# Performance work log

Measured on AMD Instinct MI355X. Metric: run time of the kernel, lower is better.

The kernel has to match this reference:

```python
import jax, jax.numpy as jnp
import numpy as np

N_NODES = 100000
N_EDGES = 3200000
IN_FEATS, N_HIDDEN, OUT_FEATS = 256, 128, 40


def setup_inputs() -> dict:
    key = jax.random.key(0)
    ks = jax.random.split(key, 8)
    x = jax.random.normal(ks[0], (N_NODES, IN_FEATS), dtype=jnp.float32)
    W0 = jax.random.normal(ks[1], (IN_FEATS, N_HIDDEN), dtype=jnp.float32) * (1.0 / np.sqrt(IN_FEATS))
    b0 = jnp.zeros((N_HIDDEN,), dtype=jnp.float32)
    W1 = jax.random.normal(ks[2], (N_HIDDEN, OUT_FEATS), dtype=jnp.float32) * (1.0 / np.sqrt(N_HIDDEN))
    b1 = jnp.zeros((OUT_FEATS,), dtype=jnp.float32)
    edge_weight = jax.random.uniform(ks[3], (N_EDGES,), dtype=jnp.float32)
    src = jax.random.randint(ks[4], (N_EDGES,), 0, N_NODES)
    dst = jax.random.randint(ks[5], (N_EDGES,), 0, N_NODES)
    return {"x": x, "W0": W0, "b0": b0, "W1": W1, "b1": b1,
            "edge_weight": edge_weight, "src": src, "dst": dst}


def reference(x, W0, b0, W1, b1, edge_weight, src, dst):
    n_nodes = x.shape[0]

    def gcn_conv(h, W, b):
        # linear transform first (PyG-style GCNConv), then sparse aggregate (SpMM)
        h = h @ W                                  # [N, d_out]
        msg = h[src] * edge_weight[:, None]        # [E, d_out] gathered + scaled
        agg = jax.ops.segment_sum(msg, dst, num_segments=n_nodes)  # scatter-add
        return agg + b

    h = jax.nn.relu(gcn_conv(x, W0, b0))
    out = gcn_conv(h, W1, b1)
    return jax.nn.log_softmax(out, axis=1)
```

## Files before the change

kernel.cpp:

```cpp
#include <hip/hip_runtime.h>
#include <hip/hip_bf16.h>
#include <cstdint>
#include <cstddef>

#define N_NODES   100000
#define N_EDGES   3200000
#define IN_FEATS  256
#define N_HIDDEN  128
#define OUT_FEATS 40

#define NB        196
#define EPB       8192
#define NBLK      391
#define HIST_M    (NB * NBLK)
#define N_TILES   3125
#define TPB       2
#define G0BLKS    ((N_TILES + TPB - 1) / TPB)

typedef __attribute__((ext_vector_type(8))) __bf16 bf16x8;
typedef __attribute__((ext_vector_type(4))) float f32x4;

#define ACC8(A_, V_, W_)                                                  \
  A_[0] = fmaf(__uint_as_float((V_).x << 16),         (W_), A_[0]);       \
  A_[1] = fmaf(__uint_as_float((V_).x & 0xFFFF0000u), (W_), A_[1]);       \
  A_[2] = fmaf(__uint_as_float((V_).y << 16),         (W_), A_[2]);       \
  A_[3] = fmaf(__uint_as_float((V_).y & 0xFFFF0000u), (W_), A_[3]);       \
  A_[4] = fmaf(__uint_as_float((V_).z << 16),         (W_), A_[4]);       \
  A_[5] = fmaf(__uint_as_float((V_).z & 0xFFFF0000u), (W_), A_[5]);       \
  A_[6] = fmaf(__uint_as_float((V_).w << 16),         (W_), A_[6]);       \
  A_[7] = fmaf(__uint_as_float((V_).w & 0xFFFF0000u), (W_), A_[7]);

__device__ __forceinline__ void gemm0_block(
    int bid, const float* __restrict__ x, const uint4* __restrict__ w0f,
    unsigned short* __restrict__ h0) {
  __shared__ __align__(16) unsigned short xb[32 * 264];
  const int tid  = threadIdx.x;
  const int lane = tid & 63;
  const int wave = tid >> 6;
  const int rb   = wave & 1;
  const int ch   = wave >> 1;
  const int l15  = lane & 15;
  const int g    = lane >> 4;

  bf16x8 Bf[4][8];
#pragma unroll
  for (int cb = 0; cb < 4; ++cb)
#pragma unroll
    for (int q = 0; q < 8; ++q)
      Bf[cb][q] = __builtin_bit_cast(bf16x8, w0f[((ch * 4 + cb) * 8 + q) * 64 + lane]);

  for (int t = 0; t < TPB; ++t) {
    const int tile = bid * TPB + t;
    if (tile >= N_TILES) break;
    const int row0 = tile * 32;
    __syncthreads();
    for (int i = tid; i < 32 * 128; i += 256) {
      const int row = i >> 7, kp = i & 127;
      const float2 v = *(const float2*)(x + (size_t)(row0 + row) * IN_FEATS + kp * 2);
      __hip_bfloat162 p;
      p.x = __float2bfloat16(v.x);
      p.y = __float2bfloat16(v.y);
      *(unsigned int*)&xb[row * 264 + kp * 2] = *(unsigned int*)&p;
    }
    __syncthreads();

    f32x4 acc[4];
#pragma unroll
    for (int cb = 0; cb < 4; ++cb) acc[cb] = (f32x4){0.f, 0.f, 0.f, 0.f};

#pragma unroll
    for (int q = 0; q < 8; ++q) {
      const bf16x8 a = *(const bf16x8*)&xb[(rb * 16 + l15) * 264 + q * 32 + g * 8];
      acc[0] = __builtin_amdgcn_mfma_f32_16x16x32_bf16(a, Bf[0][q], acc[0], 0, 0, 0);
      acc[1] = __builtin_amdgcn_mfma_f32_16x16x32_bf16(a, Bf[1][q], acc[1], 0, 0, 0);
      acc[2] = __builtin_amdgcn_mfma_f32_16x16x32_bf16(a, Bf[2][q], acc[2], 0, 0, 0);
      acc[3] = __builtin_amdgcn_mfma_f32_16x16x32_bf16(a, Bf[3][q], acc[3], 0, 0, 0);
    }

#pragma unroll
    for (int cb = 0; cb < 4; ++cb) {
      const int col = ch * 64 + cb * 16 + l15;
#pragma unroll
      for (int r = 0; r < 4; ++r) {
        const int row = row0 + rb * 16 + g * 4 + r;
        __hip_bfloat16 hb = __float2bfloat16(acc[cb][r]);
        h0[(size_t)row * N_HIDDEN + col] = *(unsigned short*)&hb;
      }
    }
  }
}

__device__ __forceinline__ void bucket_scan_block(
    int b, const int* __restrict__ bsum, int* __restrict__ histG) {
  __shared__ int sh[256];
  __shared__ int pr[256];
  const int t = threadIdx.x;

  sh[t] = (t < b) ? bsum[t] : 0;
  __syncthreads();
#pragma unroll
  for (int off = 128; off > 0; off >>= 1) {
    if (t < off) sh[t] += sh[t + off];
    __syncthreads();
  }
  const int base = sh[0];

  const int row = b * NBLK;
  const int i0 = 2 * t, i1 = 2 * t + 1;
  int a = 0, c = 0;
  if (t < 196) {
    a = histG[row + i0];
    if (i1 < NBLK) c = histG[row + i1];
  }
  pr[t] = a + c;
  __syncthreads();
  for (int off = 1; off < 256; off <<= 1) {
    int v = (t >= off) ? pr[t - off] : 0;
    __syncthreads();
    pr[t] += v;
    __syncthreads();
  }
  if (t < 196) {
    const int ebase = (t > 0) ? pr[t - 1] : 0;
    histG[row + i0] = base + ebase;
    if (i1 < NBLK) histG[row + i1] = base + ebase + a;
  }
}

__global__ __launch_bounds__(256) void bscan_gemm0_kernel(
    const int* __restrict__ bsum, int* __restrict__ histG,
    const float* __restrict__ x, const uint4* __restrict__ w0f,
    unsigned short* __restrict__ h0) {
  if (blockIdx.x < NB) bucket_scan_block(blockIdx.x, bsum, histG);
  else                 gemm0_block(blockIdx.x - NB, x, w0f, h0);
}

__global__ __launch_bounds__(256) void p1hist_kernel(
    const int* __restrict__ dst, int* __restrict__ histG,
    const float* __restrict__ W1, uint4* __restrict__ w1f,
    const float* __restrict__ W0, uint4* __restrict__ w0f,
    int* __restrict__ bsum) {
  const int tid = threadIdx.x;
  const int blk = blockIdx.x;

  if (blk >= NBLK) {
    if (blk == NBLK) {
      for (int t = tid; t < 3 * 4 * 64; t += 256) {
        const int ln  = t & 63;
        const int qq  = (t >> 6) & 3;
        const int nt  = t >> 8;
        const int l15 = ln & 15;
        const int gg  = ln >> 4;
        const int c   = nt * 16 + l15;
        const int k0  = qq * 32 + gg * 8;
        uint4 u;
        __hip_bfloat162 p;
#define W1AT(i_) ((c < OUT_FEATS) ? W1[(size_t)(k0 + (i_)) * OUT_FEATS + c] : 0.f)
        p.x = __float2bfloat16(W1AT(0)); p.y = __float2bfloat16(W1AT(1));
        u.x = *(unsigned int*)&p;
        p.x = __float2bfloat16(W1AT(2)); p.y = __float2bfloat16(W1AT(3));
        u.y = *(unsigned int*)&p;
        p.x = __float2bfloat16(W1AT(4)); p.y = __float2bfloat16(W1AT(5));
        u.z = *(unsigned int*)&p;
        p.x = __float2bfloat16(W1AT(6)); p.y = __float2bfloat16(W1AT(7));
        u.w = *(unsigned int*)&p;
#undef W1AT
        w1f[t] = u;
      }
    } else {
      const int pb = blk - NBLK - 1;
      for (int fi = pb * 512 + tid; fi < pb * 512 + 512; fi += 256) {
        const int ln  = fi & 63;
        const int qq  = (fi >> 6) & 7;
        const int ct  = fi >> 9;
        const int col = ct * 16 + (ln & 15);
        const int k0  = qq * 32 + (ln >> 4) * 8;
        uint4 u;
        __hip_bfloat162 p;
        p.x = __float2bfloat16(W0[(size_t)(k0 + 0) * N_HIDDEN + col]);
        p.y = __float2bfloat16(W0[(size_t)(k0 + 1) * N_HIDDEN + col]);
        u.x = *(unsigned int*)&p;
        p.x = __float2bfloat16(W0[(size_t)(k0 + 2) * N_HIDDEN + col]);
        p.y = __float2bfloat16(W0[(size_t)(k0 + 3) * N_HIDDEN + col]);
        u.y = *(unsigned int*)&p;
        p.x = __float2bfloat16(W0[(size_t)(k0 + 4) * N_HIDDEN + col]);
        p.y = __float2bfloat16(W0[(size_t)(k0 + 5) * N_HIDDEN + col]);
        u.z = *(unsigned int*)&p;
        p.x = __float2bfloat16(W0[(size_t)(k0 + 6) * N_HIDDEN + col]);
        p.y = __float2bfloat16(W0[(size_t)(k0 + 7) * N_HIDDEN + col]);
        u.w = *(unsigned int*)&p;
        w0f[fi] = u;
      }
    }
    return;
  }

  __shared__ int lh[NB];
  for (int i = tid; i < NB; i += 256) lh[i] = 0;
  __syncthreads();

  const int e0 = blk * EPB;
  const int e1 = min(e0 + EPB, N_EDGES);
  for (int i = e0 + tid; i < e1; i += 256)
    atomicAdd(&lh[dst[i] >> 9], 1);
  __syncthreads();

  for (int i = tid; i < NB; i += 256) {
    histG[i * NBLK + blk] = lh[i];
    atomicAdd(&bsum[i], lh[i]);
  }
}

__global__ __launch_bounds__(256) void p1scatter_kernel(
    const int* __restrict__ src, const int* __restrict__ dst,
    const float* __restrict__ ew, const int* __restrict__ histG,
    uint2* __restrict__ bucketed) {
  __shared__ uint2 stage[EPB];
  __shared__ unsigned char sbkt[EPB];
  __shared__ int lcnt[NB];
  __shared__ int lbase[NB];
  __shared__ int spart[256];
  const int tid = threadIdx.x;
  const int blk = blockIdx.x;
  const int e0 = blk * EPB;
  const int e1 = min(e0 + EPB, N_EDGES);

  for (int i = tid; i < NB; i += 256) lcnt[i] = 0;
  __syncthreads();

  for (int i = e0 + tid; i < e1; i += 256)
    atomicAdd(&lcnt[dst[i] >> 9], 1);
  __syncthreads();

  const int myv = (tid < NB) ? lcnt[tid] : 0;
  spart[tid] = myv;
  __syncthreads();
  for (int off = 1; off < 256; off <<= 1) {
    int u = (tid >= off) ? spart[tid - off] : 0;
    __syncthreads();
    spart[tid] += u;
    __syncthreads();
  }
  if (tid < NB) { lbase[tid] = spart[tid] - myv; lcnt[tid] = spart[tid] - myv; }
  __syncthreads();

  for (int i = e0 + tid; i < e1; i += 256) {
    const int d = dst[i];
    const int b = d >> 9;
    const int pos = atomicAdd(&lcnt[b], 1);
    stage[pos] = make_uint2((unsigned)src[i] | ((unsigned)(d & 511) << 17),
                            __float_as_uint(ew[i]));
    sbkt[pos] = (unsigned char)b;
  }
  __syncthreads();

  const int n = e1 - e0;
  for (int i = tid; i < n; i += 256) {
    const int b = sbkt[i];
    const int gpos = histG[b * NBLK + blk] + (i - lbase[b]);
    bucketed[gpos] = stage[i];
  }
}

__global__ __launch_bounds__(256) void p2place_kernel(
    const uint2* __restrict__ bucketed, const int* __restrict__ histG,
    int* __restrict__ offsets, int2* __restrict__ srcw) {
  __shared__ int cnt[512];
  __shared__ int part[256];
  const int t = threadIdx.x;
  const int b = blockIdx.x;
  const int node0 = b << 9;
  const int beg = histG[b * NBLK];
  const int end = (b == NB - 1) ? N_EDGES : histG[(b + 1) * NBLK];

  cnt[t] = 0; cnt[t + 256] = 0;
  __syncthreads();

  for (int j = beg + t; j < end; j += 256)
    atomicAdd(&cnt[bucketed[j].x >> 17], 1);
  __syncthreads();

  const int a0 = cnt[2 * t];
  const int a1 = cnt[2 * t + 1];
  part[t] = a0 + a1;
  __syncthreads();
  for (int off = 1; off < 256; off <<= 1) {
    int v = (t >= off) ? part[t - off] : 0;
    __syncthreads();
    part[t] += v;
    __syncthreads();
  }
  const int base = (t > 0) ? part[t - 1] : 0;

  const int o0 = beg + base;
  const int o1 = o0 + a0;
  cnt[2 * t]     = o0;
  cnt[2 * t + 1] = o1;
  const int n0 = node0 + 2 * t;
  if (n0 < N_NODES)     offsets[n0]     = o0;
  if (n0 + 1 < N_NODES) offsets[n0 + 1] = o1;
  if (b == NB - 1 && t == 0) offsets[N_NODES] = N_EDGES;
  __syncthreads();

  for (int j = beg + t; j < end; j += 256) {
    const uint2 en = bucketed[j];
    const int slot = atomicAdd(&cnt[en.x >> 17], 1);
    srcw[slot] = make_int2((int)(en.x & 0x1FFFFu), (int)en.y);
  }
}

__global__ __launch_bounds__(256) void gather0_gemm1_kernel(
    const uint4* __restrict__ h0q, const int2* __restrict__ srcw,
    const int* __restrict__ offsets, const float* __restrict__ b0,
    const uint4* __restrict__ w1f, unsigned short* __restrict__ h1a,
    unsigned short* __restrict__ h1c) {
  __shared__ float hs[4][N_HIDDEN];
  const int wave = threadIdx.x >> 6;
  const int lane = threadIdx.x & 63;
  const int node = blockIdx.x * 4 + wave;
  const int q    = lane >> 4;
  const int fl   = lane & 15;

  const int beg = __builtin_amdgcn_readfirstlane(offsets[node]);
  const int end = __builtin_amdgcn_readfirstlane(offsets[node + 1]);

  float acc[8] = {0.f, 0.f, 0.f, 0.f, 0.f, 0.f, 0.f, 0.f};

  if (end > beg) {
    const int e1 = end - 1;
    int2 sA = srcw[min(beg + q, e1)];
    int2 sB = srcw[min(beg + 4 + q, e1)];
    for (int j = beg; j < end; j += 8) {
      const float wA = (j + q < end)     ? __int_as_float(sA.y) : 0.f;
      const float wB = (j + 4 + q < end) ? __int_as_float(sB.y) : 0.f;
      const uint4 vA = h0q[(size_t)(unsigned)sA.x * 16 + fl];
      const uint4 vB = h0q[(size_t)(unsigned)sB.x * 16 + fl];
      const int jn = j + 8;
      if (jn < end) {
        sA = srcw[min(jn + q, e1)];
        sB = srcw[min(jn + 4 + q, e1)];
      }
      ACC8(acc, vA, wA)
      ACC8(acc, vB, wB)
    }
  }

#pragma unroll
  for (int i = 0; i < 8; ++i) {
    acc[i] += __shfl_xor(acc[i], 16);
    acc[i] += __shfl_xor(acc[i], 32);
  }

  if (q == 0) {
    const int f0 = fl * 8;
    float t[8];
#pragma unroll
    for (int i = 0; i < 8; ++i) {
      const float v = acc[i] + b0[f0 + i];
      t[i] = v > 0.f ? v : 0.f;
    }
    *(float4*)&hs[wave][f0]     = make_float4(t[0], t[1], t[2], t[3]);
    *(float4*)&hs[wave][f0 + 4] = make_float4(t[4], t[5], t[6], t[7]);
  }
  __syncthreads();

  if (wave < 3) {
    const int l15 = lane & 15;
    const int g   = lane >> 4;
    f32x4 c = {0.f, 0.f, 0.f, 0.f};
#pragma unroll
    for (int qq = 0; qq < 4; ++qq) {
      uint4 ua = make_uint4(0, 0, 0, 0);
      if (l15 < 4) {
        const float* hrow = &hs[l15][qq * 32 + g * 8];
        __hip_bfloat162 p;
        p.x = __float2bfloat16(hrow[0]); p.y = __float2bfloat16(hrow[1]);
        ua.x = *(unsigned int*)&p;
        p.x = __float2bfloat16(hrow[2]); p.y = __float2bfloat16(hrow[3]);
        ua.y = *(unsigned int*)&p;
        p.x = __float2bfloat16(hrow[4]); p.y = __float2bfloat16(hrow[5]);
        ua.z = *(unsigned int*)&p;
        p.x = __float2bfloat16(hrow[6]); p.y = __float2bfloat16(hrow[7]);
        ua.w = *(unsigned int*)&p;
      }
      const uint4 ub = w1f[(wave * 4 + qq) * 64 + lane];
      c = __builtin_amdgcn_mfma_f32_16x16x32_bf16(
            __builtin_bit_cast(bf16x8, ua), __builtin_bit_cast(bf16x8, ub),
            c, 0, 0, 0);
    }
    if (g == 0) {
#pragma unroll
      for (int r = 0; r < 4; ++r) {
        const int nodeR = blockIdx.x * 4 + r;
        const int f = wave * 16 + l15;
        __hip_bfloat16 hb = __float2bfloat16(c[r]);
        const unsigned short v16 = *(unsigned short*)&hb;
        if (f < 32)              h1a[(size_t)nodeR * 32 + f] = v16;
        else if (f < OUT_FEATS)  h1c[(size_t)nodeR * 8 + (f - 32)] = v16;
      }
    }
  }
}

__global__ __launch_bounds__(256) void gather1_lsm_kernel(
    const uint4* __restrict__ h1aq, const uint4* __restrict__ h1cq,
    const int2* __restrict__ srcw, const int* __restrict__ offsets,
    const float* __restrict__ b1, float* __restrict__ out) {
  const int wave = threadIdx.x >> 6;
  const int lane = threadIdx.x & 63;
  const int node = blockIdx.x * 4 + wave;
  const int g  = lane >> 2;
  const int fl = lane & 3;

  const int beg = __builtin_amdgcn_readfirstlane(offsets[node]);
  const int end = __builtin_amdgcn_readfirstlane(offsets[node + 1]);

  float acc[8]  = {0.f, 0.f, 0.f, 0.f, 0.f, 0.f, 0.f, 0.f};
  float acc2[8] = {0.f, 0.f, 0.f, 0.f, 0.f, 0.f, 0.f, 0.f};

  if (end > beg) {
    const int e1 = end - 1;
    int2 sA = srcw[min(beg + g, e1)];
    int2 sB = srcw[min(beg + 16 + g, e1)];
    for (int j = beg; j < end; j += 32) {
      const float wA = (j + g < end)      ? __int_as_float(sA.y) : 0.f;
      const float wB = (j + 16 + g < end) ? __int_as_float(sB.y) : 0.f;
      const uint4 vA = h1aq[(size_t)(unsigned)sA.x * 4 + fl];
      const uint4 vB = h1aq[(size_t)(unsigned)sB.x * 4 + fl];
      uint4 cA = make_uint4(0, 0, 0, 0), cB = make_uint4(0, 0, 0, 0);
      if (fl == 0) {
        cA = h1cq[(unsigned)sA.x];
        cB = h1cq[(unsigned)sB.x];
      }
      const int jn = j + 32;
      if (jn < end) {
        sA = srcw[min(jn + g, e1)];
        sB = srcw[min(jn + 16 + g, e1)];
      }
      ACC8(acc, vA, wA)
      ACC8(acc, vB, wB)
      if (fl == 0) {
        ACC8(acc2, cA, wA)
        ACC8(acc2, cB, wB)
      }
    }
  }

#pragma unroll
  for (int i = 0; i < 8; ++i) {
    acc[i]  += __shfl_xor(acc[i], 4);
    acc[i]  += __shfl_xor(acc[i], 8);
    acc[i]  += __shfl_xor(acc[i], 16);
    acc[i]  += __shfl_xor(acc[i], 32);
    acc2[i] += __shfl_xor(acc2[i], 4);
    acc2[i] += __shfl_xor(acc2[i], 8);
    acc2[i] += __shfl_xor(acc2[i], 16);
    acc2[i] += __shfl_xor(acc2[i], 32);
    acc2[i] += __shfl_xor(acc2[i], 1);
    acc2[i] += __shfl_xor(acc2[i], 2);
  }

  const int f0 = fl * 8;
  float m = -INFINITY;
#pragma unroll
  for (int i = 0; i < 8; ++i) {
    acc[i]  += b1[f0 + i];
    acc2[i] += b1[32 + i];
    m = fmaxf(m, acc[i]);
    m = fmaxf(m, acc2[i]);
  }
  m = fmaxf(m, __shfl_xor(m, 1));
  m = fmaxf(m, __shfl_xor(m, 2));

  float s = 0.f;
#pragma unroll
  for (int i = 0; i < 8; ++i) s += expf(acc[i] - m);
  s += __shfl_xor(s, 1);
  s += __shfl_xor(s, 2);
  float s2 = 0.f;
#pragma unroll
  for (int i = 0; i < 8; ++i) s2 += expf(acc2[i] - m);
  s += s2;

  const float lse = m + logf(s);
  if (lane < 4) {
    float* op = out + (size_t)node * OUT_FEATS + fl * 8;
    *(float4*)op       = make_float4(acc[0] - lse, acc[1] - lse,
                                     acc[2] - lse, acc[3] - lse);
    *(float4*)(op + 4) = make_float4(acc[4] - lse, acc[5] - lse,
                                     acc[6] - lse, acc[7] - lse);
  } else if (lane == 4) {
    float* op = out + (size_t)node * OUT_FEATS + 32;
    *(float4*)op       = make_float4(acc2[0] - lse, acc2[1] - lse,
                                     acc2[2] - lse, acc2[3] - lse);
    *(float4*)(op + 4) = make_float4(acc2[4] - lse, acc2[5] - lse,
                                     acc2[6] - lse, acc2[7] - lse);
  }
}

extern "C" void kernel_launch(void* const* d_in, const int* in_sizes, int n_in,
                              void* d_out, int out_size, void* d_ws, size_t ws_size,
                              hipStream_t stream) {
  const float* x   = (const float*)d_in[0];
  const float* W0  = (const float*)d_in[1];
  const float* b0  = (const float*)d_in[2];
  const float* W1  = (const float*)d_in[3];
  const float* b1  = (const float*)d_in[4];
  const float* ew  = (const float*)d_in[5];
  const int*   src = (const int*)d_in[6];
  const int*   dst = (const int*)d_in[7];
  float* out = (float*)d_out;

  char* ws = (char*)d_ws;
  unsigned int* h0b2 = (unsigned int*)(ws);
  int2*  srcw     = (int2*)(ws + 25600000);
  uint2* bucketed = (uint2*)(ws + 51200000);
  int*   offsets  = (int*)(ws + 76800000);
  int*   histG    = (int*)(ws + 77200064);
  unsigned short* h1a = (unsigned short*)(ws + 77506624);
  unsigned short* h1c = (unsigned short*)(ws + 83906624);
  uint4* w1f      = (uint4*)(ws + 85506624);
  uint4* w0f      = (uint4*)(ws + 85518912);
  int*   bsum     = (int*)(ws + 85584448);

  hipMemsetAsync(bsum, 0, NB * sizeof(int), stream);
  p1hist_kernel<<<NBLK + 9, 256, 0, stream>>>(dst, histG, W1, w1f, W0, w0f, bsum);
  bscan_gemm0_kernel<<<NB + G0BLKS, 256, 0, stream>>>(
      bsum, histG, x, w0f, (unsigned short*)h0b2);
  p1scatter_kernel<<<NBLK, 256, 0, stream>>>(src, dst, ew, histG, bucketed);
  p2place_kernel<<<NB, 256, 0, stream>>>(bucketed, histG, offsets, srcw);

  gather0_gemm1_kernel<<<N_NODES / 4, 256, 0, stream>>>(
      (const uint4*)h0b2, srcw, offsets, b0, (const uint4*)w1f, h1a, h1c);
  gather1_lsm_kernel<<<N_NODES / 4, 256, 0, stream>>>(
      (const uint4*)h1a, (const uint4*)h1c, srcw, offsets, b1, out);
}
```

Baseline: 511.2 us.

## Replace two-pass bucketed CSR build with global-atomic counting sort and packed FMA

Swaps the two-level bucket histogram/scatter/place CSR construction for a per-node global atomic histogram, a two-kernel node-level prefix scan, and a direct atomic-cursor scatter into the CSR edge array. This drops the intermediate bucketed buffer and one full pass over the edges, but relies on heavily contended global atomics and produces a nondeterministic edge order within each node. The gather kernels also switch to packed float2 FMAs, and the hidden-state LDS row is padded.

```diff
diff --git a/kernel.cpp b/kernel.cpp
--- a/kernel.cpp
+++ b/kernel.cpp
@@ -9,26 +9,28 @@
 #define N_HIDDEN  128
 #define OUT_FEATS 40
 
-#define NB        196
-#define EPB       8192
-#define NBLK      391
-#define HIST_M    (NB * NBLK)
+#define NCHUNK    391
+#define HISTB     391
 #define N_TILES   3125
 #define TPB       2
 #define G0BLKS    ((N_TILES + TPB - 1) / TPB)
 
 typedef __attribute__((ext_vector_type(8))) __bf16 bf16x8;
 typedef __attribute__((ext_vector_type(4))) float f32x4;
-
-#define ACC8(A_, V_, W_)                                                  \
-  A_[0] = fmaf(__uint_as_float((V_).x << 16),         (W_), A_[0]);       \
-  A_[1] = fmaf(__uint_as_float((V_).x & 0xFFFF0000u), (W_), A_[1]);       \
-  A_[2] = fmaf(__uint_as_float((V_).y << 16),         (W_), A_[2]);       \
-  A_[3] = fmaf(__uint_as_float((V_).y & 0xFFFF0000u), (W_), A_[3]);       \
-  A_[4] = fmaf(__uint_as_float((V_).z << 16),         (W_), A_[4]);       \
-  A_[5] = fmaf(__uint_as_float((V_).z & 0xFFFF0000u), (W_), A_[5]);       \
-  A_[6] = fmaf(__uint_as_float((V_).w << 16),         (W_), A_[6]);       \
-  A_[7] = fmaf(__uint_as_float((V_).w & 0xFFFF0000u), (W_), A_[7]);
+typedef __attribute__((ext_vector_type(2))) float f32x2;
+
+__device__ __forceinline__ void pkfma(f32x2& a, unsigned int u, f32x2 w2) {
+  f32x2 b;
+  b.x = __uint_as_float(u << 16);
+  b.y = __uint_as_float(u & 0xFFFF0000u);
+  a += b * w2;
+}
+
+#define ACC8P(A_, V_, W2_)   \
+  pkfma(A_[0], (V_).x, W2_); \
+  pkfma(A_[1], (V_).y, W2_); \
+  pkfma(A_[2], (V_).z, W2_); \
+  pkfma(A_[3], (V_).w, W2_);
 
 __device__ __forceinline__ void gemm0_block(
     int bid, const float* __restrict__ x, const uint4* __restrict__ w0f,
@@ -90,61 +92,15 @@
   }
 }
 
-__device__ __forceinline__ void bucket_scan_block(
-    int b, const int* __restrict__ bsum, int* __restrict__ histG) {
-  __shared__ int sh[256];
-  __shared__ int pr[256];
-  const int t = threadIdx.x;
-
-  sh[t] = (t < b) ? bsum[t] : 0;
-  __syncthreads();
-#pragma unroll
-  for (int off = 128; off > 0; off >>= 1) {
-    if (t < off) sh[t] += sh[t + off];
-    __syncthreads();
-  }
-  const int base = sh[0];
-
-  const int row = b * NBLK;
-  const int i0 = 2 * t, i1 = 2 * t + 1;
-  int a = 0, c = 0;
-  if (t < 196) {
-    a = histG[row + i0];
-    if (i1 < NBLK) c = histG[row + i1];
-  }
-  pr[t] = a + c;
-  __syncthreads();
-  for (int off = 1; off < 256; off <<= 1) {
-    int v = (t >= off) ? pr[t - off] : 0;
-    __syncthreads();
-    pr[t] += v;
-    __syncthreads();
-  }
-  if (t < 196) {
-    const int ebase = (t > 0) ? pr[t - 1] : 0;
-    histG[row + i0] = base + ebase;
-    if (i1 < NBLK) histG[row + i1] = base + ebase + a;
-  }
-}
-
-__global__ __launch_bounds__(256) void bscan_gemm0_kernel(
-    const int* __restrict__ bsum, int* __restrict__ histG,
-    const float* __restrict__ x, const uint4* __restrict__ w0f,
-    unsigned short* __restrict__ h0) {
-  if (blockIdx.x < NB) bucket_scan_block(blockIdx.x, bsum, histG);
-  else                 gemm0_block(blockIdx.x - NB, x, w0f, h0);
-}
-
-__global__ __launch_bounds__(256) void p1hist_kernel(
-    const int* __restrict__ dst, int* __restrict__ histG,
+__global__ __launch_bounds__(256) void hist_prep_kernel(
+    const int* __restrict__ dst, int* __restrict__ cnt,
     const float* __restrict__ W1, uint4* __restrict__ w1f,
-    const float* __restrict__ W0, uint4* __restrict__ w0f,
-    int* __restrict__ bsum) {
+    const float* __restrict__ W0, uint4* __restrict__ w0f) {
   const int tid = threadIdx.x;
   const int blk = blockIdx.x;
 
-  if (blk >= NBLK) {
-    if (blk == NBLK) {
+  if (blk >= HISTB) {
+    if (blk == HISTB) {
       for (int t = tid; t < 3 * 4 * 64; t += 256) {
         const int ln  = t & 63;
         const int qq  = (t >> 6) & 3;
@@ -168,7 +124,7 @@
         w1f[t] = u;
       }
     } else {
-      const int pb = blk - NBLK - 1;
+      const int pb = blk - HISTB - 1;
       for (int fi = pb * 512 + tid; fi < pb * 512 + 512; fi += 256) {
         const int ln  = fi & 63;
         const int qq  = (fi >> 6) & 7;
@@ -195,117 +151,78 @@
     return;
   }
 
-  __shared__ int lh[NB];
-  for (int i = tid; i < NB; i += 256) lh[i] = 0;
+#pragma unroll 4
+  for (int i = blk * 256 + tid; i < N_EDGES; i += HISTB * 256)
+    atomicAdd(&cnt[dst[i]], 1);
+}
+
+__global__ __launch_bounds__(256) void psum_kernel(
+    const int* __restrict__ cnt, int* __restrict__ psum) {
+  __shared__ int sh[256];
+  const int b = blockIdx.x, t = threadIdx.x;
+  const int n = b * 256 + t;
+  sh[t] = (n < N_NODES) ? cnt[n] : 0;
   __syncthreads();
-
-  const int e0 = blk * EPB;
-  const int e1 = min(e0 + EPB, N_EDGES);
-  for (int i = e0 + tid; i < e1; i += 256)
-    atomicAdd(&lh[dst[i] >> 9], 1);
+#pragma unroll
+  for (int off = 128; off > 0; off >>= 1) {
+    if (t < off) sh[t] += sh[t + off];
+    __syncthreads();
+  }
+  if (t == 0) psum[b] = sh[0];
+}
+
+__device__ __forceinline__ void node_scan_block(
+    int b, const int* __restrict__ cnt, const int* __restrict__ psum,
+    int* __restrict__ offsets, int* __restrict__ curs) {
+  __shared__ int sh[256];
+  __shared__ int pr[256];
+  const int t = threadIdx.x;
+
+  int v = (t < b) ? psum[t] : 0;
+  if (t + 256 < b) v += psum[t + 256];
+  sh[t] = v;
   __syncthreads();
-
-  for (int i = tid; i < NB; i += 256) {
-    histG[i * NBLK + blk] = lh[i];
-    atomicAdd(&bsum[i], lh[i]);
-  }
-}
-
-__global__ __launch_bounds__(256) void p1scatter_kernel(
-    const int* __restrict__ src, const int* __restrict__ dst,
-    const float* __restrict__ ew, const int* __restrict__ histG,
-    uint2* __restrict__ bucketed) {
-  __shared__ uint2 stage[EPB];
-  __shared__ unsigned char sbkt[EPB];
-  __shared__ int lcnt[NB];
-  __shared__ int lbase[NB];
-  __shared__ int spart[256];
-  const int tid = threadIdx.x;
-  const int blk = blockIdx.x;
-  const int e0 = blk * EPB;
-  const int e1 = min(e0 + EPB, N_EDGES);
-
-  for (int i = tid; i < NB; i += 256) lcnt[i] = 0;
-  __syncthreads();
-
-  for (int i = e0 + tid; i < e1; i += 256)
-    atomicAdd(&lcnt[dst[i] >> 9], 1);
-  __syncthreads();
-
-  const int myv = (tid < NB) ? lcnt[tid] : 0;
-  spart[tid] = myv;
+#pragma unroll
+  for (int off = 128; off > 0; off >>= 1) {
+    if (t < off) sh[t] += sh[t + off];
+    __syncthreads();
+  }
+  const int base = sh[0];
+
+  const int node = b * 256 + t;
+  const int c = (node < N_NODES) ? cnt[node] : 0;
+  pr[t] = c;
   __syncthreads();
   for (int off = 1; off < 256; off <<= 1) {
-    int u = (tid >= off) ? spart[tid - off] : 0;
-    __syncthreads();
-    spart[tid] += u;
-    __syncthreads();
-  }
-  if (tid < NB) { lbase[tid] = spart[tid] - myv; lcnt[tid] = spart[tid] - myv; }
-  __syncthreads();
-
-  for (int i = e0 + tid; i < e1; i += 256) {
+    int u = (t >= off) ? pr[t - off] : 0;
+    __syncthreads();
+    pr[t] += u;
+    __syncthreads();
+  }
+  const int excl = base + pr[t] - c;
+  if (node < N_NODES) { offsets[node] = excl; curs[node] = excl; }
+  if (b == NCHUNK - 1 && t == 255) offsets[N_NODES] = base + pr[255];
+}
+
+__global__ __launch_bounds__(256) void nscan_gemm0_kernel(
+    const int* __restrict__ cnt, const int* __restrict__ psum,
+    int* __restrict__ offsets, int* __restrict__ curs,
+    const float* __restrict__ x, const uint4* __restrict__ w0f,
+    unsigned short* __restrict__ h0) {
+  if (blockIdx.x < NCHUNK) node_scan_block(blockIdx.x, cnt, psum, offsets, curs);
+  else                     gemm0_block(blockIdx.x - NCHUNK, x, w0f, h0);
+}
+
+__global__ __launch_bounds__(256) void scatter_kernel(
+    const int* __restrict__ src, const int* __restrict__ dst,
+    const float* __restrict__ ew, int* __restrict__ curs,
+    int2* __restrict__ srcw) {
+#pragma unroll 4
+  for (int i = blockIdx.x * 256 + threadIdx.x; i < N_EDGES;
+       i += gridDim.x * 256) {
     const int d = dst[i];
-    const int b = d >> 9;
-    const int pos = atomicAdd(&lcnt[b], 1);
-    stage[pos] = make_uint2((unsigned)src[i] | ((unsigned)(d & 511) << 17),
-                            __float_as_uint(ew[i]));
-    sbkt[pos] = (unsigned char)b;
-  }
-  __syncthreads();
-
-  const int n = e1 - e0;
-  for (int i = tid; i < n; i += 256) {
-    const int b = sbkt[i];
-    const int gpos = histG[b * NBLK + blk] + (i - lbase[b]);
-    bucketed[gpos] = stage[i];
-  }
-}
-
-__global__ __launch_bounds__(256) void p2place_kernel(
-    const uint2* __restrict__ bucketed, const int* __restrict__ histG,
-    int* __restrict__ offsets, int2* __restrict__ srcw) {
-  __shared__ int cnt[512];
-  __shared__ int part[256];
-  const int t = threadIdx.x;
-  const int b = blockIdx.x;
-  const int node0 = b << 9;
-  const int beg = histG[b * NBLK];
-  const int end = (b == NB - 1) ? N_EDGES : histG[(b + 1) * NBLK];
-
-  cnt[t] = 0; cnt[t + 256] = 0;
-  __syncthreads();
-
-  for (int j = beg + t; j < end; j += 256)
-    atomicAdd(&cnt[bucketed[j].x >> 17], 1);
-  __syncthreads();
-
-  const int a0 = cnt[2 * t];
-  const int a1 = cnt[2 * t + 1];
-  part[t] = a0 + a1;
-  __syncthreads();
-  for (int off = 1; off < 256; off <<= 1) {
-    int v = (t >= off) ? part[t - off] : 0;
-    __syncthreads();
-    part[t] += v;
-    __syncthreads();
-  }
-  const int base = (t > 0) ? part[t - 1] : 0;
-
-  const int o0 = beg + base;
-  const int o1 = o0 + a0;
-  cnt[2 * t]     = o0;
-  cnt[2 * t + 1] = o1;
-  const int n0 = node0 + 2 * t;
-  if (n0 < N_NODES)     offsets[n0]     = o0;
-  if (n0 + 1 < N_NODES) offsets[n0 + 1] = o1;
-  if (b == NB - 1 && t == 0) offsets[N_NODES] = N_EDGES;
-  __syncthreads();
-
-  for (int j = beg + t; j < end; j += 256) {
-    const uint2 en = bucketed[j];
-    const int slot = atomicAdd(&cnt[en.x >> 17], 1);
-    srcw[slot] = make_int2((int)(en.x & 0x1FFFFu), (int)en.y);
+    const int pos = atomicAdd(&curs[d], 1);
+    srcw[pos] = make_int2(src[i], __float_as_int(ew[i]));
   }
 }
 
@@ -314,7 +231,7 @@
     const int* __restrict__ offsets, const float* __restrict__ b0,
     const uint4* __restrict__ w1f, unsigned short* __restrict__ h1a,
     unsigned short* __restrict__ h1c) {
-  __shared__ float hs[4][N_HIDDEN];
+  __shared__ float hs[4][132];
   const int wave = threadIdx.x >> 6;
   const int lane = threadIdx.x & 63;
   const int node = blockIdx.x * 4 + wave;
@@ -324,7 +241,9 @@
   const int beg = __builtin_amdgcn_readfirstlane(offsets[node]);
   const int end = __builtin_amdgcn_readfirstlane(offsets[node + 1]);
 
-  float acc[8] = {0.f, 0.f, 0.f, 0.f, 0.f, 0.f, 0.f, 0.f};
+  f32x2 acc[4];
+#pragma unroll
+  for (int i = 0; i < 4; ++i) acc[i] = (f32x2){0.f, 0.f};
 
   if (end > beg) {
     const int e1 = end - 1;
@@ -333,6 +252,8 @@
     for (int j = beg; j < end; j += 8) {
       const float wA = (j + q < end)     ? __int_as_float(sA.y) : 0.f;
       const float wB = (j + 4 + q < end) ? __int_as_float(sB.y) : 0.f;
+      const f32x2 w2A = {wA, wA};
+      const f32x2 w2B = {wB, wB};
       const uint4 vA = h0q[(size_t)(unsigned)sA.x * 16 + fl];
       const uint4 vB = h0q[(size_t)(unsigned)sB.x * 16 + fl];
       const int jn = j + 8;
@@ -340,15 +261,17 @@
         sA = srcw[min(jn + q, e1)];
         sB = srcw[min(jn + 4 + q, e1)];
       }
-      ACC8(acc, vA, wA)
-      ACC8(acc, vB, wB)
-    }
-  }
-
-#pragma unroll
-  for (int i = 0; i < 8; ++i) {
-    acc[i] += __shfl_xor(acc[i], 16);
-    acc[i] += __shfl_xor(acc[i], 32);
+      ACC8P(acc, vA, w2A)
+      ACC8P(acc, vB, w2B)
+    }
+  }
+
+#pragma unroll
+  for (int i = 0; i < 4; ++i) {
+    acc[i].x += __shfl_xor(acc[i].x, 16);
+    acc[i].x += __shfl_xor(acc[i].x, 32);
+    acc[i].y += __shfl_xor(acc[i].y, 16);
+    acc[i].y += __shfl_xor(acc[i].y, 32);
   }
 
   if (q == 0) {
@@ -356,7 +279,8 @@
     float t[8];
 #pragma unroll
     for (int i = 0; i < 8; ++i) {
-      const float v = acc[i] + b0[f0 + i];
+      const float a = ((i & 1) ? acc[i >> 1].y : acc[i >> 1].x);
+      const float v = a + b0[f0 + i];
       t[i] = v > 0.f ? v : 0.f;
     }
     *(float4*)&hs[wave][f0]     = make_float4(t[0], t[1], t[2], t[3]);
@@ -415,8 +339,9 @@
   const int beg = __builtin_amdgcn_readfirstlane(offsets[node]);
   const int end = __builtin_amdgcn_readfirstlane(offsets[node + 1]);
 
-  float acc[8]  = {0.f, 0.f, 0.f, 0.f, 0.f, 0.f, 0.f, 0.f};
-  float acc2[8] = {0.f, 0.f, 0.f, 0.f, 0.f, 0.f, 0.f, 0.f};
+  f32x2 a1[4], a2[4];
+#pragma unroll
+  for (int i = 0; i < 4; ++i) { a1[i] = (f32x2){0.f, 0.f}; a2[i] = (f32x2){0.f, 0.f}; }
 
   if (end > beg) {
     const int e1 = end - 1;
@@ -425,6 +350,8 @@
     for (int j = beg; j < end; j += 32) {
       const float wA = (j + g < end)      ? __int_as_float(sA.y) : 0.f;
       const float wB = (j + 16 + g < end) ? __int_as_float(sB.y) : 0.f;
+      const f32x2 w2A = {wA, wA};
+      const f32x2 w2B = {wB, wB};
       const uint4 vA = h1aq[(size_t)(unsigned)sA.x * 4 + fl];
       const uint4 vB = h1aq[(size_t)(unsigned)sB.x * 4 + fl];
       uint4 cA = make_uint4(0, 0, 0, 0), cB = make_uint4(0, 0, 0, 0);
@@ -437,64 +364,68 @@
         sA = srcw[min(jn + g, e1)];
         sB = srcw[min(jn + 16 + g, e1)];
       }
-      ACC8(acc, vA, wA)
-      ACC8(acc, vB, wB)
+      ACC8P(a1, vA, w2A)
+      ACC8P(a1, vB, w2B)
       if (fl == 0) {
-        ACC8(acc2, cA, wA)
-        ACC8(acc2, cB, wB)
-      }
-    }
-  }
-
-#pragma unroll
-  for (int i = 0; i < 8; ++i) {
-    acc[i]  += __shfl_xor(acc[i], 4);
-    acc[i]  += __shfl_xor(acc[i], 8);
-    acc[i]  += __shfl_xor(acc[i], 16);
-    acc[i]  += __shfl_xor(acc[i], 32);
-    acc2[i] += __shfl_xor(acc2[i], 4);
-    acc2[i] += __shfl_xor(acc2[i], 8);
-    acc2[i] += __shfl_xor(acc2[i], 16);
-    acc2[i] += __shfl_xor(acc2[i], 32);
-    acc2[i] += __shfl_xor(acc2[i], 1);
-    acc2[i] += __shfl_xor(acc2[i], 2);
+        ACC8P(a2, cA, w2A)
+        ACC8P(a2, cB, w2B)
+      }
+    }
+  }
+
+  float o[8], o2[8];
+#pragma unroll
+  for (int i = 0; i < 4; ++i) {
+    float x0 = a1[i].x, y0 = a1[i].y, x2 = a2[i].x, y2 = a2[i].y;
+    x0 += __shfl_xor(x0, 4);  x0 += __shfl_xor(x0, 8);
+    x0 += __shfl_xor(x0, 16); x0 += __shfl_xor(x0, 32);
+    y0 += __shfl_xor(y0, 4);  y0 += __shfl_xor(y0, 8);
+    y0 += __shfl_xor(y0, 16); y0 += __shfl_xor(y0, 32);
+    x2 += __shfl_xor(x2, 4);  x2 += __shfl_xor(x2, 8);
+    x2 += __shfl_xor(x2, 16); x2 += __shfl_xor(x2, 32);
+    x2 += __shfl_xor(x2, 1);  x2 += __shfl_xor(x2, 2);
+    y2 += __shfl_xor(y2, 4);  y2 += __shfl_xor(y2, 8);
+    y2 += __shfl_xor(y2, 16); y2 += __shfl_xor(y2, 32);
+    y2 += __shfl_xor(y2, 1);  y2 += __shfl_xor(y2, 2);
+    o[2 * i] = x0; o[2 * i + 1] = y0;
+    o2[2 * i] = x2; o2[2 * i + 1] = y2;
   }
 
   const int f0 = fl * 8;
   float m = -INFINITY;
 #pragma unroll
   for (int i = 0; i < 8; ++i) {
-    acc[i]  += b1[f0 + i];
-    acc2[i] += b1[32 + i];
-    m = fmaxf(m, acc[i]);
-    m = fmaxf(m, acc2[i]);
+    o[i]  += b1[f0 + i];
+    o2[i] += b1[32 + i];
+    m = fmaxf(m, o[i]);
+    m = fmaxf(m, o2[i]);
   }
   m = fmaxf(m, __shfl_xor(m, 1));
   m = fmaxf(m, __shfl_xor(m, 2));
 
   float s = 0.f;
 #pragma unroll
-  for (int i = 0; i < 8; ++i) s += expf(acc[i] - m);
+  for (int i = 0; i < 8; ++i) s += expf(o[i] - m);
   s += __shfl_xor(s, 1);
   s += __shfl_xor(s, 2);
   float s2 = 0.f;
 #pragma unroll
-  for (int i = 0; i < 8; ++i) s2 += expf(acc2[i] - m);
+  for (int i = 0; i < 8; ++i) s2 += expf(o2[i] - m);
   s += s2;
 
   const float lse = m + logf(s);
   if (lane < 4) {
     float* op = out + (size_t)node * OUT_FEATS + fl * 8;
-    *(float4*)op       = make_float4(acc[0] - lse, acc[1] - lse,
-                                     acc[2] - lse, acc[3] - lse);
-    *(float4*)(op + 4) = make_float4(acc[4] - lse, acc[5] - lse,
-                                     acc[6] - lse, acc[7] - lse);
+    *(float4*)op       = make_float4(o[0] - lse, o[1] - lse,
+                                     o[2] - lse, o[3] - lse);
+    *(float4*)(op + 4) = make_float4(o[4] - lse, o[5] - lse,
+                                     o[6] - lse, o[7] - lse);
   } else if (lane == 4) {
     float* op = out + (size_t)node * OUT_FEATS + 32;
-    *(float4*)op       = make_float4(acc2[0] - lse, acc2[1] - lse,
-                                     acc2[2] - lse, acc2[3] - lse);
-    *(float4*)(op + 4) = make_float4(acc2[4] - lse, acc2[5] - lse,
-                                     acc2[6] - lse, acc2[7] - lse);
+    *(float4*)op       = make_float4(o2[0] - lse, o2[1] - lse,
+                                     o2[2] - lse, o2[3] - lse);
+    *(float4*)(op + 4) = make_float4(o2[4] - lse, o2[5] - lse,
+                                     o2[6] - lse, o2[7] - lse);
   }
 }
 
@@ -513,22 +444,22 @@
 
   char* ws = (char*)d_ws;
   unsigned int* h0b2 = (unsigned int*)(ws);
-  int2*  srcw     = (int2*)(ws + 25600000);
-  uint2* bucketed = (uint2*)(ws + 51200000);
-  int*   offsets  = (int*)(ws + 76800000);
-  int*   histG    = (int*)(ws + 77200064);
-  unsigned short* h1a = (unsigned short*)(ws + 77506624);
-  unsigned short* h1c = (unsigned short*)(ws + 83906624);
-  uint4* w1f      = (uint4*)(ws + 85506624);
-  uint4* w0f      = (uint4*)(ws + 85518912);
-  int*   bsum     = (int*)(ws + 85584448);
-
-  hipMemsetAsync(bsum, 0, NB * sizeof(int), stream);
-  p1hist_kernel<<<NBLK + 9, 256, 0, stream>>>(dst, histG, W1, w1f, W0, w0f, bsum);
-  bscan_gemm0_kernel<<<NB + G0BLKS, 256, 0, stream>>>(
-      bsum, histG, x, w0f, (unsigned short*)h0b2);
-  p1scatter_kernel<<<NBLK, 256, 0, stream>>>(src, dst, ew, histG, bucketed);
-  p2place_kernel<<<NB, 256, 0, stream>>>(bucketed, histG, offsets, srcw);
+  int2* srcw     = (int2*)(ws + 25600000);
+  int*  offsets  = (int*)(ws + 51200000);
+  int*  cnt      = (int*)(ws + 51600016);
+  int*  curs     = (int*)(ws + 52000016);
+  int*  psum     = (int*)(ws + 52400016);
+  unsigned short* h1a = (unsigned short*)(ws + 52401600);
+  unsigned short* h1c = (unsigned short*)(ws + 58801600);
+  uint4* w1f     = (uint4*)(ws + 60401600);
+  uint4* w0f     = (uint4*)(ws + 60413888);
+
+  hipMemsetAsync(cnt, 0, N_NODES * sizeof(int), stream);
+  hist_prep_kernel<<<HISTB + 9, 256, 0, stream>>>(dst, cnt, W1, w1f, W0, w0f);
+  psum_kernel<<<NCHUNK, 256, 0, stream>>>(cnt, psum);
+  nscan_gemm0_kernel<<<NCHUNK + G0BLKS, 256, 0, stream>>>(
+      cnt, psum, offsets, curs, x, w0f, (unsigned short*)h0b2);
+  scatter_kernel<<<782, 256, 0, stream>>>(src, dst, ew, curs, srcw);
 
   gather0_gemm1_kernel<<<N_NODES / 4, 256, 0, stream>>>(
       (const uint4*)h0b2, srcw, offsets, b0, (const uint4*)w1f, h1a, h1c);
```

Result: slower. 796.4 us (+55.8%).
